# Performance work log

Hardware: AMD Instinct MI355X
Metric: run time of the kernel (lower is better)

The kernel has to match this reference:

```python
import jax, jax.numpy as jnp
import numpy as np

D = 256
H = 16
HD = D // H
N_BIAS = 6
B, E = 8, 1024


def _layernorm(x, g, b, eps=1e-5):
    mu = jnp.mean(x, axis=-1, keepdims=True)
    var = jnp.mean(jnp.square(x - mu), axis=-1, keepdims=True)
    return (x - mu) * jax.lax.rsqrt(var + eps) * g + b


def setup_inputs() -> dict:
    key = jax.random.key(0)
    ks = jax.random.split(key, 16)
    s = 0.02
    inp = {
        "x": jax.random.normal(ks[0], (B, E, D), dtype=jnp.float32),
        "struct_bias": jax.random.randint(ks[1], (B, E, E), 0, N_BIAS),
        "key_padding_mask": jnp.zeros((B, E), dtype=bool),
        # projections stored as [in, out] so y = x @ W + b
        "Wq": jax.random.normal(ks[2], (D, D), jnp.float32) * s,
        "bq": jnp.zeros((D,), jnp.float32),
        "Wk": jax.random.normal(ks[3], (D, D), jnp.float32) * s,
        "bk": jnp.zeros((D,), jnp.float32),
        "Wv": jax.random.normal(ks[4], (D, D), jnp.float32) * s,
        "bv": jnp.zeros((D,), jnp.float32),
        "Wo": jax.random.normal(ks[5], (D, D), jnp.float32) * s,
        "bo": jnp.zeros((D,), jnp.float32),
        "bias_emb": jax.random.normal(ks[6], (N_BIAS, H), jnp.float32) * s,
        "ln1_g": jnp.ones((D,), jnp.float32),
        "ln1_b": jnp.zeros((D,), jnp.float32),
        "W_ff1": jax.random.normal(ks[7], (D, 4 * D), jnp.float32) * s,
        "b_ff1": jnp.zeros((4 * D,), jnp.float32),
        "W_ff2": jax.random.normal(ks[8], (4 * D, D), jnp.float32) * s,
        "b_ff2": jnp.zeros((D,), jnp.float32),
        "ln2_g": jnp.ones((D,), jnp.float32),
        "ln2_b": jnp.zeros((D,), jnp.float32),
    }
    return inp


def reference(x, struct_bias, key_padding_mask, Wq, bq, Wk, bk, Wv, bv, Wo, bo,
              bias_emb, ln1_g, ln1_b, W_ff1, b_ff1, W_ff2, b_ff2, ln2_g, ln2_b):
    b, e, d = x.shape
    # project and split heads: [B, H, E, HD]
    q = (x @ Wq + bq).reshape(b, e, H, HD).transpose(0, 2, 1, 3)
    k = (x @ Wk + bk).reshape(b, e, H, HD).transpose(0, 2, 1, 3)
    v = (x @ Wv + bv).reshape(b, e, H, HD).transpose(0, 2, 1, 3)
    scores = jnp.einsum('bhqd,bhkd->bhqk', q, k) / np.sqrt(HD).astype(np.float32)
    # learned structural bias: [B,E,E,H] -> [B,H,E,E]
    bias = bias_emb[struct_bias].transpose(0, 3, 1, 2)
    scores = scores + bias
    scores = jnp.where(key_padding_mask[:, None, None, :], -jnp.inf, scores)
    attn = jax.nn.softmax(scores, axis=-1)
    out = jnp.einsum('bhqk,bhkd->bhqd', attn, v)
    out = out.transpose(0, 2, 1, 3).reshape(b, e, d)
    out = out @ Wo + bo
    x = _layernorm(x + out, ln1_g, ln1_b)
    ff = jax.nn.gelu(x @ W_ff1 + b_ff1, approximate=False) @ W_ff2 + b_ff2
    x = _layernorm(x + ff, ln2_g, ln2_b)
    return x
```

## Files before the change

### kernel.cpp

```cpp
#include <hip/hip_runtime.h>
#include <math.h>

#define B_  8
#define E_  1024
#define D_  256
#define H_  16
#define FF_ 1024
#define M_  (B_ * E_)

typedef __attribute__((ext_vector_type(8))) short short8;
typedef __attribute__((ext_vector_type(4))) float f32x4;
typedef unsigned short bf16u;

#define GLOAD_LDS16(g, l) __builtin_amdgcn_global_load_lds( \
    (const __attribute__((address_space(1))) void*)(g), \
    (__attribute__((address_space(3))) void*)(l), 16, 0, 0)

__device__ __forceinline__ unsigned short f2bf(float f) {
  union { float f; unsigned u; } c; c.f = f;
  unsigned r = c.u + 0x7fffu + ((c.u >> 16) & 1u);
  return (unsigned short)(r >> 16);
}
__device__ __forceinline__ float gelu_exact(float x) {
  return 0.5f * x * (1.0f + erff(x * 0.70710678118654752f));
}

template<int BM, int BN, int EPI>
__global__ __launch_bounds__(256) void mm_k(
    const bf16u* __restrict__ A, const bf16u* __restrict__ Wt,
    const float* __restrict__ bias, const float* __restrict__ R,
    void* __restrict__ Cout, int M, int N, int K)
{
  constexpr int WM = BM / 2, WN = BN / 2;
  constexpr int MT = WM / 16, NT = WN / 16;
  constexpr int PA = BM * 8 / 256, PB = BN * 8 / 256;
  constexpr int LBM = (BM == 128 ? 7 : 6), LBN = (BN == 128 ? 7 : 6);
  __shared__ bf16u As[BM * 64];
  __shared__ bf16u Bs[BN * 64];

  const int t = threadIdx.x;
  const int l15 = t & 15, quad = (t >> 4) & 3;
  const int w = t >> 6, wm = w >> 1, wn = w & 1;
  const int m0 = blockIdx.x * BM, n0 = blockIdx.y * BN;

  f32x4 acc[MT][NT];
  const f32x4 z4 = {0.f, 0.f, 0.f, 0.f};
#pragma unroll
  for (int i = 0; i < MT; ++i)
#pragma unroll
    for (int j = 0; j < NT; ++j) acc[i][j] = z4;

  for (int k0 = 0; k0 < K; k0 += 64) {
    __syncthreads();
#pragma unroll
    for (int p = 0; p < PA; ++p) {
      int g = p * 256 + t;
      int m = g & (BM - 1), c = g >> LBM;
      const bf16u* src = A + (size_t)(m0 + m) * K + k0 + c * 8;
      GLOAD_LDS16(src, As + g * 8);
    }
#pragma unroll
    for (int p = 0; p < PB; ++p) {
      int g = p * 256 + t;
      int n = g & (BN - 1), c = g >> LBN;
      const bf16u* src = Wt + (size_t)(n0 + n) * K + k0 + c * 8;
      GLOAD_LDS16(src, Bs + g * 8);
    }
    __syncthreads();
#pragma unroll
    for (int s = 0; s < 2; ++s) {
      short8 af[MT], bfr[NT];
#pragma unroll
      for (int mt = 0; mt < MT; ++mt)
        af[mt] = *(const short8*)(As + ((s * 4 + quad) * BM + wm * WM + mt * 16 + l15) * 8);
#pragma unroll
      for (int nt = 0; nt < NT; ++nt)
        bfr[nt] = *(const short8*)(Bs + ((s * 4 + quad) * BN + wn * WN + nt * 16 + l15) * 8);
#pragma unroll
      for (int mt = 0; mt < MT; ++mt)
#pragma unroll
        for (int nt = 0; nt < NT; ++nt)
          acc[mt][nt] = __builtin_amdgcn_mfma_f32_16x16x32_bf16(
              af[mt], bfr[nt], acc[mt][nt], 0, 0, 0);
    }
  }

#pragma unroll
  for (int mt = 0; mt < MT; ++mt) {
#pragma unroll
    for (int nt = 0; nt < NT; ++nt) {
      int col = n0 + wn * WN + nt * 16 + l15;
      float bia = bias[col];
#pragma unroll
      for (int r = 0; r < 4; ++r) {
        int row = m0 + wm * WM + mt * 16 + quad * 4 + r;
        size_t idx = (size_t)row * N + col;
        float v = acc[mt][nt][r] + bia;
        if (EPI == 1)      { ((float*)Cout)[idx] = v + R[idx]; }
        else if (EPI == 2) { ((bf16u*)Cout)[idx] = f2bf(gelu_exact(v)); }
        else               { ((bf16u*)Cout)[idx] = f2bf(v); }
      }
    }
  }
}

__global__ __launch_bounds__(256) void tcvt4_k(
    const float* __restrict__ s0, const float* __restrict__ s1,
    const float* __restrict__ s2, const float* __restrict__ s3,
    bf16u* __restrict__ d0, bf16u* __restrict__ d1,
    bf16u* __restrict__ d2, bf16u* __restrict__ d3)
{
  const int z = blockIdx.z;
  const float* src = (z == 0) ? s0 : (z == 1) ? s1 : (z == 2) ? s2 : s3;
  bf16u* dst = (z == 0) ? d0 : (z == 1) ? d1 : (z == 2) ? d2 : d3;
  __shared__ float tile[32][33];
  const int tx = threadIdx.x & 31, ty = threadIdx.x >> 5;
  const int kb = blockIdx.x * 32, nb = blockIdx.y * 32;
#pragma unroll
  for (int r = 0; r < 4; ++r)
    tile[ty + 8 * r][tx] = src[(size_t)(kb + ty + 8 * r) * 256 + nb + tx];
  __syncthreads();
#pragma unroll
  for (int r = 0; r < 4; ++r)
    dst[(size_t)(nb + ty + 8 * r) * 256 + kb + tx] = f2bf(tile[tx][ty + 8 * r]);
}

__global__ __launch_bounds__(256) void tcvt_k(const float* __restrict__ src,
    bf16u* __restrict__ dst, int K, int N)
{
  __shared__ float tile[32][33];
  const int tx = threadIdx.x & 31, ty = threadIdx.x >> 5;
  const int kb = blockIdx.x * 32, nb = blockIdx.y * 32;
#pragma unroll
  for (int r = 0; r < 4; ++r)
    tile[ty + 8 * r][tx] = src[(size_t)(kb + ty + 8 * r) * N + nb + tx];
  __syncthreads();
#pragma unroll
  for (int r = 0; r < 4; ++r)
    dst[(size_t)(nb + ty + 8 * r) * K + kb + tx] = f2bf(tile[tx][ty + 8 * r]);
}

__global__ __launch_bounds__(256) void cvt_k(const float* __restrict__ X,
    bf16u* __restrict__ Y)
{
  int i = blockIdx.x * 256 + threadIdx.x;
  float4 a = ((const float4*)X)[i * 2];
  float4 b = ((const float4*)X)[i * 2 + 1];
  uint4 o;
  o.x = f2bf(a.x) | ((unsigned)f2bf(a.y) << 16);
  o.y = f2bf(a.z) | ((unsigned)f2bf(a.w) << 16);
  o.z = f2bf(b.x) | ((unsigned)f2bf(b.y) << 16);
  o.w = f2bf(b.z) | ((unsigned)f2bf(b.w) << 16);
  ((uint4*)Y)[i] = o;
}

__global__ void bcat_k(const float* __restrict__ bq, const float* __restrict__ bk,
                       const float* __restrict__ bv, float* __restrict__ o)
{
  int i = blockIdx.x * 256 + threadIdx.x;
  o[i] = (i < 256) ? bq[i] : (i < 512) ? bk[i - 256] : bv[i - 512];
}

__global__ __launch_bounds__(256) void attn_k(
    const bf16u* __restrict__ qkv, const int* __restrict__ sb,
    const unsigned char* __restrict__ mask, const float* __restrict__ be,
    bf16u* __restrict__ O)
{
  __shared__ bf16u Kl[2][64][40];
  __shared__ bf16u Vt[2][16][72];
  __shared__ bf16u Pl[4][16][40];
  __shared__ float embl[2][6];

  const int t    = threadIdx.x;
  const int b    = blockIdx.z;
  const int hg   = blockIdx.y;
  const int w    = t >> 6;
  const int lane = t & 63;
  const int l15  = lane & 15;
  const int quad = lane >> 4;
  const int q0w  = blockIdx.x * 64 + w * 16;

  if (t < 12) embl[t / 6][t % 6] = be[(t % 6) * 16 + hg * 2 + t / 6];

  {
    float4 z = {0.f, 0.f, 0.f, 0.f};
    float4* kp = (float4*)&Kl[0][0][0];
    for (int i = t; i < 640; i += 256) kp[i] = z;
  }

  short8 qf[2];
#pragma unroll
  for (int hp = 0; hp < 2; ++hp) {
    uint4 v = {0u, 0u, 0u, 0u};
    if (quad < 2)
      v = *(const uint4*)(qkv + ((size_t)(b * E_) + q0w + l15) * 768 +
                          (hg * 2 + hp) * 16 + quad * 8);
    else if (quad == 2)
      v.x = 0x3F80u;
    union { uint4 u; short8 s; } c; c.u = v;
    qf[hp] = c.s;
  }

  const int s_hp   = t >> 7;
  const int s_key  = (t >> 1) & 63;
  const int s_half = t & 1;
  const size_t kvbase = (size_t)b * E_ * 768;
  const int* sbp = sb + ((size_t)b * E_ + q0w) * E_;

  f32x4 accO[2];
  const f32x4 z4 = {0.f, 0.f, 0.f, 0.f};
  accO[0] = z4; accO[1] = z4;
  float lsum[2][4] = {};

  for (int k0 = 0; k0 < E_; k0 += 64) {
    int sbv[2][2][4];
#pragma unroll
    for (int s2 = 0; s2 < 2; ++s2)
#pragma unroll
      for (int f = 0; f < 2; ++f)
#pragma unroll
        for (int r = 0; r < 4; ++r)
          sbv[s2][f][r] = sbp[(size_t)(quad * 4 + r) * E_ + k0 + s2 * 32 + f * 16 + l15];

    __syncthreads();
    {
      const bf16u* kq = qkv + kvbase + (size_t)(k0 + s_key) * 768 + 256 +
                        (hg * 2 + s_hp) * 16 + s_half * 8;
      uint4 kw = *(const uint4*)kq;
      uint4 vw = *(const uint4*)(kq + 256);
      *(uint4*)&Kl[s_hp][s_key][s_half * 8] = kw;
      const int col = (s_key >> 5) * 32 + ((s_key & 15) << 1) + ((s_key >> 4) & 1);
      union { uint4 u; bf16u e[8]; } vc; vc.u = vw;
#pragma unroll
      for (int j = 0; j < 8; ++j)
        Vt[s_hp][s_half * 8 + j][col] = vc.e[j];
      if (s_half == 0) {
        unsigned char mv = mask[b * E_ + k0 + s_key];
        Kl[s_hp][s_key][16] = mv ? (bf16u)0xCF6E : (bf16u)0;
      }
    }
    __syncthreads();

#pragma unroll
    for (int hp = 0; hp < 2; ++hp) {
#pragma unroll
      for (int s2 = 0; s2 < 2; ++s2) {
        short8 kf0 = *(const short8*)&Kl[hp][s2 * 32 + l15][quad * 8];
        short8 kf1 = *(const short8*)&Kl[hp][s2 * 32 + 16 + l15][quad * 8];
        f32x4 sc0 = __builtin_amdgcn_mfma_f32_16x16x32_bf16(qf[hp], kf0, z4, 0, 0, 0);
        f32x4 sc1 = __builtin_amdgcn_mfma_f32_16x16x32_bf16(qf[hp], kf1, z4, 0, 0, 0);
#pragma unroll
        for (int r = 0; r < 4; ++r) {
          float w0 = embl[hp][sbv[s2][0][r]];
          float w1 = embl[hp][sbv[s2][1][r]];
          float p0 = __expf(fmaf(sc0[r], 0.25f, w0));
          float p1 = __expf(fmaf(sc1[r], 0.25f, w1));
          unsigned u0 = __float_as_uint(p0) & 0xffff0000u;
          unsigned u1 = __float_as_uint(p1) & 0xffff0000u;
          lsum[hp][r] += __uint_as_float(u0) + __uint_as_float(u1);
          *(unsigned*)&Pl[w][quad * 4 + r][l15 * 2] = (__float_as_uint(p0) >> 16) | u1;
        }
        short8 pf = *(const short8*)&Pl[w][l15][quad * 8];
        short8 vf = *(const short8*)&Vt[hp][l15][s2 * 32 + quad * 8];
        accO[hp] = __builtin_amdgcn_mfma_f32_16x16x32_bf16(pf, vf, accO[hp], 0, 0, 0);
      }
    }
  }

#pragma unroll
  for (int off = 1; off <= 8; off <<= 1)
#pragma unroll
    for (int hp = 0; hp < 2; ++hp)
#pragma unroll
      for (int r = 0; r < 4; ++r)
        lsum[hp][r] += __shfl_xor(lsum[hp][r], off, 64);

#pragma unroll
  for (int hp = 0; hp < 2; ++hp) {
#pragma unroll
    for (int r = 0; r < 4; ++r) {
      float o = accO[hp][r] / lsum[hp][r];
      O[((size_t)(b * E_) + q0w + quad * 4 + r) * 256 + (hg * 2 + hp) * 16 + l15] = f2bf(o);
    }
  }
}

template<int DUAL>
__global__ __launch_bounds__(256) void ln_k(
    const float* __restrict__ X, const float* __restrict__ g,
    const float* __restrict__ bta, float* __restrict__ Y, bf16u* __restrict__ Yb)
{
  const int row  = blockIdx.x * 4 + (threadIdx.x >> 6);
  const int lane = threadIdx.x & 63;
  float4 v = *(const float4*)(X + (size_t)row * D_ + lane * 4);
  float s  = v.x + v.y + v.z + v.w;
  float ss = v.x * v.x + v.y * v.y + v.z * v.z + v.w * v.w;
#pragma unroll
  for (int off = 32; off; off >>= 1) {
    s  += __shfl_xor(s, off, 64);
    ss += __shfl_xor(ss, off, 64);
  }
  float mu  = s * (1.f / 256.f);
  float var = ss * (1.f / 256.f) - mu * mu;
  float rs  = 1.f / sqrtf(var + 1e-5f);
  float4 gv = *(const float4*)(g + lane * 4);
  float4 bv = *(const float4*)(bta + lane * 4);
  float4 o;
  o.x = (v.x - mu) * rs * gv.x + bv.x;
  o.y = (v.y - mu) * rs * gv.y + bv.y;
  o.z = (v.z - mu) * rs * gv.z + bv.z;
  o.w = (v.w - mu) * rs * gv.w + bv.w;
  *(float4*)(Y + (size_t)row * D_ + lane * 4) = o;
  if (DUAL) {
    uint2 p;
    p.x = f2bf(o.x) | ((unsigned)f2bf(o.y) << 16);
    p.y = f2bf(o.z) | ((unsigned)f2bf(o.w) << 16);
    *(uint2*)(Yb + (size_t)row * D_ + lane * 4) = p;
  }
}

extern "C" void kernel_launch(void* const* d_in, const int* in_sizes, int n_in,
                              void* d_out, int out_size, void* d_ws, size_t ws_size,
                              hipStream_t stream) {
  const float* x   = (const float*)d_in[0];
  const int*   sb  = (const int*)d_in[1];
  const unsigned char* mask = (const unsigned char*)d_in[2];
  const float* Wq  = (const float*)d_in[3];
  const float* bq  = (const float*)d_in[4];
  const float* Wk  = (const float*)d_in[5];
  const float* bk  = (const float*)d_in[6];
  const float* Wv  = (const float*)d_in[7];
  const float* bv  = (const float*)d_in[8];
  const float* Wo  = (const float*)d_in[9];
  const float* bo  = (const float*)d_in[10];
  const float* be  = (const float*)d_in[11];
  const float* g1  = (const float*)d_in[12];
  const float* b1  = (const float*)d_in[13];
  const float* Wf1 = (const float*)d_in[14];
  const float* bf1 = (const float*)d_in[15];
  const float* Wf2 = (const float*)d_in[16];
  const float* bf2 = (const float*)d_in[17];
  const float* g2  = (const float*)d_in[18];
  const float* b2  = (const float*)d_in[19];
  float* out = (float*)d_out;

  char* ws = (char*)d_ws;
  bf16u* Wqkvt = (bf16u*)(ws + 0);
  bf16u* Wot   = (bf16u*)(ws + 393216);
  bf16u* Wf1t  = (bf16u*)(ws + 524288);
  bf16u* Wf2t  = (bf16u*)(ws + 1048576);
  float* bqkv  = (float*)(ws + 1572864);
  bf16u* xb    = (bf16u*)(ws + 2097152);
  bf16u* qkv   = (bf16u*)(ws + 6291456);
  bf16u* att   = (bf16u*)(ws + 18874368);
  float* t1    = (float*)(ws + 23068672);
  float* x1    = (float*)(ws + 31457280);
  bf16u* x1b   = (bf16u*)(ws + 39845888);
  bf16u* ffh   = (bf16u*)(ws + 2097152);
  float* t2    = (float*)(ws + 18874368);

  dim3 blk(256);

  tcvt4_k<<<dim3(8, 8, 4), blk, 0, stream>>>(Wq, Wk, Wv, Wo,
      Wqkvt, Wqkvt + 65536, Wqkvt + 131072, Wot);
  tcvt_k<<<dim3(8, 32), blk, 0, stream>>>(Wf1, Wf1t, 256, 1024);
  tcvt_k<<<dim3(32, 8), blk, 0, stream>>>(Wf2, Wf2t, 1024, 256);
  bcat_k<<<3, blk, 0, stream>>>(bq, bk, bv, bqkv);
  cvt_k<<<1024, blk, 0, stream>>>(x, xb);

  mm_k<128, 128, 0><<<dim3(64, 6), blk, 0, stream>>>(xb, Wqkvt, bqkv, nullptr,
                                                     qkv, M_, 768, 256);
  attn_k<<<dim3(16, 8, 8), blk, 0, stream>>>(qkv, sb, mask, be, att);

  mm_k<64, 64, 1><<<dim3(128, 4), blk, 0, stream>>>(att, Wot, bo, x,
                                                    t1, M_, 256, 256);
  ln_k<1><<<M_ / 4, blk, 0, stream>>>(t1, g1, b1, x1, x1b);

  mm_k<128, 128, 2><<<dim3(64, 8), blk, 0, stream>>>(x1b, Wf1t, bf1, nullptr,
                                                     ffh, M_, 1024, 256);
  mm_k<64, 64, 1><<<dim3(128, 4), blk, 0, stream>>>(ffh, Wf2t, bf2, x1,
                                                    t2, M_, 256, 1024);
  ln_k<0><<<M_ / 4, blk, 0, stream>>>(t2, g2, b2, out, nullptr);
}
```

Measured before the change: 239.0 us.

## Pack struct bias to bytes, split attention per head, use exp2, retile QKV GEMM

A conversion pass now packs the int32 structural-bias indices into uint8, and the attention kernel reads those bytes. This cuts the dominant bias read traffic, which is otherwise repeated for every head group. The attention kernel now handles one head per block instead of two, which doubles the grid and shares K/V loading between thread halves. The exponent is folded into exp2 with prescaled constants. The QKV GEMM tile is halved in M. The one-head-per-block split means the bias bytes are re-read 16 times instead of 8, trading more repeated reads for more parallelism.

After: 248.2 us. 3.9% more time.

```diff
diff --git a/kernel.cpp b/kernel.cpp
--- a/kernel.cpp
+++ b/kernel.cpp
@@ -141,17 +141,29 @@
 }
 
 __global__ __launch_bounds__(256) void cvt_k(const float* __restrict__ X,
-    bf16u* __restrict__ Y)
-{
-  int i = blockIdx.x * 256 + threadIdx.x;
-  float4 a = ((const float4*)X)[i * 2];
-  float4 b = ((const float4*)X)[i * 2 + 1];
-  uint4 o;
-  o.x = f2bf(a.x) | ((unsigned)f2bf(a.y) << 16);
-  o.y = f2bf(a.z) | ((unsigned)f2bf(a.w) << 16);
-  o.z = f2bf(b.x) | ((unsigned)f2bf(b.y) << 16);
-  o.w = f2bf(b.z) | ((unsigned)f2bf(b.w) << 16);
-  ((uint4*)Y)[i] = o;
+    bf16u* __restrict__ Y, const int* __restrict__ sb,
+    unsigned char* __restrict__ sbb)
+{
+  const int bid = blockIdx.x;
+  if (bid < 1024) {
+    int i = bid * 256 + threadIdx.x;
+    float4 a = ((const float4*)X)[i * 2];
+    float4 b = ((const float4*)X)[i * 2 + 1];
+    uint4 o;
+    o.x = f2bf(a.x) | ((unsigned)f2bf(a.y) << 16);
+    o.y = f2bf(a.z) | ((unsigned)f2bf(a.w) << 16);
+    o.z = f2bf(b.x) | ((unsigned)f2bf(b.y) << 16);
+    o.w = f2bf(b.z) | ((unsigned)f2bf(b.w) << 16);
+    ((uint4*)Y)[i] = o;
+  } else {
+    int i = (bid - 1024) * 256 + threadIdx.x;
+    int4 a = ((const int4*)sb)[i * 2];
+    int4 c = ((const int4*)sb)[i * 2 + 1];
+    uint2 o;
+    o.x = (unsigned)a.x | ((unsigned)a.y << 8) | ((unsigned)a.z << 16) | ((unsigned)a.w << 24);
+    o.y = (unsigned)c.x | ((unsigned)c.y << 8) | ((unsigned)c.z << 16) | ((unsigned)c.w << 24);
+    ((uint2*)sbb)[i] = o;
+  }
 }
 
 __global__ void bcat_k(const float* __restrict__ bq, const float* __restrict__ bk,
@@ -162,55 +174,54 @@
 }
 
 __global__ __launch_bounds__(256) void attn_k(
-    const bf16u* __restrict__ qkv, const int* __restrict__ sb,
+    const bf16u* __restrict__ qkv, const unsigned char* __restrict__ sbb,
     const unsigned char* __restrict__ mask, const float* __restrict__ be,
     bf16u* __restrict__ O)
 {
-  __shared__ bf16u Kl[2][64][40];
-  __shared__ bf16u Vt[2][16][72];
+  __shared__ bf16u Kl[64][40];
+  __shared__ bf16u Vt[16][74];
   __shared__ bf16u Pl[4][16][40];
-  __shared__ float embl[2][6];
+  __shared__ float embl[6];
 
   const int t    = threadIdx.x;
   const int b    = blockIdx.z;
-  const int hg   = blockIdx.y;
+  const int h    = blockIdx.y;
   const int w    = t >> 6;
   const int lane = t & 63;
   const int l15  = lane & 15;
   const int quad = lane >> 4;
   const int q0w  = blockIdx.x * 64 + w * 16;
-
-  if (t < 12) embl[t / 6][t % 6] = be[(t % 6) * 16 + hg * 2 + t / 6];
+  const float C2 = 0.36067376022224085f;
+
+  if (t < 6) embl[t] = be[t * 16 + h] * 1.44269504088896f;
 
   {
     float4 z = {0.f, 0.f, 0.f, 0.f};
-    float4* kp = (float4*)&Kl[0][0][0];
-    for (int i = t; i < 640; i += 256) kp[i] = z;
-  }
-
-  short8 qf[2];
-#pragma unroll
-  for (int hp = 0; hp < 2; ++hp) {
+    float4* kp = (float4*)&Kl[0][0];
+    for (int i = t; i < 320; i += 256) kp[i] = z;
+  }
+
+  short8 qf;
+  {
     uint4 v = {0u, 0u, 0u, 0u};
     if (quad < 2)
       v = *(const uint4*)(qkv + ((size_t)(b * E_) + q0w + l15) * 768 +
-                          (hg * 2 + hp) * 16 + quad * 8);
+                          h * 16 + quad * 8);
     else if (quad == 2)
       v.x = 0x3F80u;
     union { uint4 u; short8 s; } c; c.u = v;
-    qf[hp] = c.s;
-  }
-
-  const int s_hp   = t >> 7;
+    qf = c.s;
+  }
+
   const int s_key  = (t >> 1) & 63;
   const int s_half = t & 1;
   const size_t kvbase = (size_t)b * E_ * 768;
-  const int* sbp = sb + ((size_t)b * E_ + q0w) * E_;
-
-  f32x4 accO[2];
+  const unsigned char* sbp = sbb + ((size_t)(b * E_) + q0w) * E_;
+
+  f32x4 accO;
   const f32x4 z4 = {0.f, 0.f, 0.f, 0.f};
-  accO[0] = z4; accO[1] = z4;
-  float lsum[2][4] = {};
+  accO = z4;
+  float lsum[4] = {};
 
   for (int k0 = 0; k0 < E_; k0 += 64) {
     int sbv[2][2][4];
@@ -224,64 +235,58 @@
 
     __syncthreads();
     {
-      const bf16u* kq = qkv + kvbase + (size_t)(k0 + s_key) * 768 + 256 +
-                        (hg * 2 + s_hp) * 16 + s_half * 8;
-      uint4 kw = *(const uint4*)kq;
-      uint4 vw = *(const uint4*)(kq + 256);
-      *(uint4*)&Kl[s_hp][s_key][s_half * 8] = kw;
-      const int col = (s_key >> 5) * 32 + ((s_key & 15) << 1) + ((s_key >> 4) & 1);
-      union { uint4 u; bf16u e[8]; } vc; vc.u = vw;
-#pragma unroll
-      for (int j = 0; j < 8; ++j)
-        Vt[s_hp][s_half * 8 + j][col] = vc.e[j];
-      if (s_half == 0) {
-        unsigned char mv = mask[b * E_ + k0 + s_key];
-        Kl[s_hp][s_key][16] = mv ? (bf16u)0xCF6E : (bf16u)0;
+      const bf16u* base = qkv + kvbase + (size_t)(k0 + s_key) * 768 +
+                          h * 16 + s_half * 8;
+      if (t < 128) {
+        *(uint4*)&Kl[s_key][s_half * 8] = *(const uint4*)(base + 256);
+        if (t < 64) {
+          unsigned char mv = mask[b * E_ + k0 + t];
+          Kl[t][16] = mv ? (bf16u)0xCF6E : (bf16u)0;
+        }
+      } else {
+        uint4 vw = *(const uint4*)(base + 512);
+        const int col = (s_key >> 5) * 32 + ((s_key & 15) << 1) + ((s_key >> 4) & 1);
+        union { uint4 u; bf16u e[8]; } vc; vc.u = vw;
+#pragma unroll
+        for (int j = 0; j < 8; ++j)
+          Vt[s_half * 8 + j][col] = vc.e[j];
       }
     }
     __syncthreads();
 
 #pragma unroll
-    for (int hp = 0; hp < 2; ++hp) {
-#pragma unroll
-      for (int s2 = 0; s2 < 2; ++s2) {
-        short8 kf0 = *(const short8*)&Kl[hp][s2 * 32 + l15][quad * 8];
-        short8 kf1 = *(const short8*)&Kl[hp][s2 * 32 + 16 + l15][quad * 8];
-        f32x4 sc0 = __builtin_amdgcn_mfma_f32_16x16x32_bf16(qf[hp], kf0, z4, 0, 0, 0);
-        f32x4 sc1 = __builtin_amdgcn_mfma_f32_16x16x32_bf16(qf[hp], kf1, z4, 0, 0, 0);
-#pragma unroll
-        for (int r = 0; r < 4; ++r) {
-          float w0 = embl[hp][sbv[s2][0][r]];
-          float w1 = embl[hp][sbv[s2][1][r]];
-          float p0 = __expf(fmaf(sc0[r], 0.25f, w0));
-          float p1 = __expf(fmaf(sc1[r], 0.25f, w1));
-          unsigned u0 = __float_as_uint(p0) & 0xffff0000u;
-          unsigned u1 = __float_as_uint(p1) & 0xffff0000u;
-          lsum[hp][r] += __uint_as_float(u0) + __uint_as_float(u1);
-          *(unsigned*)&Pl[w][quad * 4 + r][l15 * 2] = (__float_as_uint(p0) >> 16) | u1;
-        }
-        short8 pf = *(const short8*)&Pl[w][l15][quad * 8];
-        short8 vf = *(const short8*)&Vt[hp][l15][s2 * 32 + quad * 8];
-        accO[hp] = __builtin_amdgcn_mfma_f32_16x16x32_bf16(pf, vf, accO[hp], 0, 0, 0);
+    for (int s2 = 0; s2 < 2; ++s2) {
+      short8 kf0 = *(const short8*)&Kl[s2 * 32 + l15][quad * 8];
+      short8 kf1 = *(const short8*)&Kl[s2 * 32 + 16 + l15][quad * 8];
+      f32x4 sc0 = __builtin_amdgcn_mfma_f32_16x16x32_bf16(qf, kf0, z4, 0, 0, 0);
+      f32x4 sc1 = __builtin_amdgcn_mfma_f32_16x16x32_bf16(qf, kf1, z4, 0, 0, 0);
+#pragma unroll
+      for (int r = 0; r < 4; ++r) {
+        float w0 = embl[sbv[s2][0][r]];
+        float w1 = embl[sbv[s2][1][r]];
+        float p0 = __builtin_amdgcn_exp2f(fmaf(sc0[r], C2, w0));
+        float p1 = __builtin_amdgcn_exp2f(fmaf(sc1[r], C2, w1));
+        unsigned u0 = __float_as_uint(p0) & 0xffff0000u;
+        unsigned u1 = __float_as_uint(p1) & 0xffff0000u;
+        lsum[r] += __uint_as_float(u0) + __uint_as_float(u1);
+        *(unsigned*)&Pl[w][quad * 4 + r][l15 * 2] = (__float_as_uint(p0) >> 16) | u1;
       }
+      short8 pf = *(const short8*)&Pl[w][l15][quad * 8];
+      short8 vf = *(const short8*)&Vt[l15][s2 * 32 + quad * 8];
+      accO = __builtin_amdgcn_mfma_f32_16x16x32_bf16(pf, vf, accO, 0, 0, 0);
     }
   }
 
 #pragma unroll
   for (int off = 1; off <= 8; off <<= 1)
 #pragma unroll
-    for (int hp = 0; hp < 2; ++hp)
-#pragma unroll
-      for (int r = 0; r < 4; ++r)
-        lsum[hp][r] += __shfl_xor(lsum[hp][r], off, 64);
-
-#pragma unroll
-  for (int hp = 0; hp < 2; ++hp) {
-#pragma unroll
-    for (int r = 0; r < 4; ++r) {
-      float o = accO[hp][r] / lsum[hp][r];
-      O[((size_t)(b * E_) + q0w + quad * 4 + r) * 256 + (hg * 2 + hp) * 16 + l15] = f2bf(o);
-    }
+    for (int r = 0; r < 4; ++r)
+      lsum[r] += __shfl_xor(lsum[r], off, 64);
+
+#pragma unroll
+  for (int r = 0; r < 4; ++r) {
+    float o = accO[r] / lsum[r];
+    O[((size_t)(b * E_) + q0w + quad * 4 + r) * 256 + h * 16 + l15] = f2bf(o);
   }
 }
 
@@ -353,6 +358,7 @@
   bf16u* xb    = (bf16u*)(ws + 2097152);
   bf16u* qkv   = (bf16u*)(ws + 6291456);
   bf16u* att   = (bf16u*)(ws + 18874368);
+  unsigned char* sbb = (unsigned char*)(ws + 23068672);
   float* t1    = (float*)(ws + 23068672);
   float* x1    = (float*)(ws + 31457280);
   bf16u* x1b   = (bf16u*)(ws + 39845888);
@@ -366,11 +372,11 @@
   tcvt_k<<<dim3(8, 32), blk, 0, stream>>>(Wf1, Wf1t, 256, 1024);
   tcvt_k<<<dim3(32, 8), blk, 0, stream>>>(Wf2, Wf2t, 1024, 256);
   bcat_k<<<3, blk, 0, stream>>>(bq, bk, bv, bqkv);
-  cvt_k<<<1024, blk, 0, stream>>>(x, xb);
-
-  mm_k<128, 128, 0><<<dim3(64, 6), blk, 0, stream>>>(xb, Wqkvt, bqkv, nullptr,
+  cvt_k<<<5120, blk, 0, stream>>>(x, xb, sb, sbb);
+
+  mm_k<64, 128, 0><<<dim3(128, 6), blk, 0, stream>>>(xb, Wqkvt, bqkv, nullptr,
                                                      qkv, M_, 768, 256);
-  attn_k<<<dim3(16, 8, 8), blk, 0, stream>>>(qkv, sb, mask, be, att);
+  attn_k<<<dim3(16, 16, 8), blk, 0, stream>>>(qkv, sbb, mask, be, att);
 
   mm_k<64, 64, 1><<<dim3(128, 4), blk, 0, stream>>>(att, Wot, bo, x,
                                                     t1, M_, 256, 256);
```

## Fuse prep kernels, pack struct bias to bytes, double-buffer attention K/V loads

Applied to the files above, without the earlier changes.

Merges the five small weight/bias/input conversion kernels into one prep kernel, which also packs the int32 structural-bias indices into bytes so the attention kernel reads a quarter of the bytes for the dominant B*E*E stream. The attention loop becomes register-prefetched and double-buffered in LDS with one barrier per iteration. It also folds log2e into the scale and embeddings to use exp2, swizzles K in LDS, pads V, and sets a min-blocks launch bound. The packing pass adds a full read of the int32 index tensor each call, the larger LDS footprint may reduce occupancy, and the byte buffer reuses workspace later used for t1.

Measured after the change: 316.4 us. 32.4% more time.

```diff
diff --git a/kernel.cpp b/kernel.cpp
--- a/kernel.cpp
+++ b/kernel.cpp
@@ -104,70 +104,76 @@
   }
 }
 
-__global__ __launch_bounds__(256) void tcvt4_k(
-    const float* __restrict__ s0, const float* __restrict__ s1,
-    const float* __restrict__ s2, const float* __restrict__ s3,
-    bf16u* __restrict__ d0, bf16u* __restrict__ d1,
-    bf16u* __restrict__ d2, bf16u* __restrict__ d3)
-{
-  const int z = blockIdx.z;
-  const float* src = (z == 0) ? s0 : (z == 1) ? s1 : (z == 2) ? s2 : s3;
-  bf16u* dst = (z == 0) ? d0 : (z == 1) ? d1 : (z == 2) ? d2 : d3;
-  __shared__ float tile[32][33];
-  const int tx = threadIdx.x & 31, ty = threadIdx.x >> 5;
-  const int kb = blockIdx.x * 32, nb = blockIdx.y * 32;
-#pragma unroll
-  for (int r = 0; r < 4; ++r)
-    tile[ty + 8 * r][tx] = src[(size_t)(kb + ty + 8 * r) * 256 + nb + tx];
-  __syncthreads();
-#pragma unroll
-  for (int r = 0; r < 4; ++r)
-    dst[(size_t)(nb + ty + 8 * r) * 256 + kb + tx] = f2bf(tile[tx][ty + 8 * r]);
-}
-
-__global__ __launch_bounds__(256) void tcvt_k(const float* __restrict__ src,
-    bf16u* __restrict__ dst, int K, int N)
+__global__ __launch_bounds__(256) void prep_k(
+    const float* __restrict__ Wq, const float* __restrict__ Wk,
+    const float* __restrict__ Wv, const float* __restrict__ Wo,
+    const float* __restrict__ Wf1, const float* __restrict__ Wf2,
+    bf16u* __restrict__ Wqkvt, bf16u* __restrict__ Wot,
+    bf16u* __restrict__ Wf1t, bf16u* __restrict__ Wf2t,
+    const float* __restrict__ bq, const float* __restrict__ bk,
+    const float* __restrict__ bv, float* __restrict__ bqkv,
+    const float* __restrict__ X, bf16u* __restrict__ Xb,
+    const int* __restrict__ sb, unsigned char* __restrict__ sbb)
 {
   __shared__ float tile[32][33];
-  const int tx = threadIdx.x & 31, ty = threadIdx.x >> 5;
-  const int kb = blockIdx.x * 32, nb = blockIdx.y * 32;
-#pragma unroll
-  for (int r = 0; r < 4; ++r)
-    tile[ty + 8 * r][tx] = src[(size_t)(kb + ty + 8 * r) * N + nb + tx];
-  __syncthreads();
-#pragma unroll
-  for (int r = 0; r < 4; ++r)
-    dst[(size_t)(nb + ty + 8 * r) * K + kb + tx] = f2bf(tile[tx][ty + 8 * r]);
-}
-
-__global__ __launch_bounds__(256) void cvt_k(const float* __restrict__ X,
-    bf16u* __restrict__ Y)
-{
-  int i = blockIdx.x * 256 + threadIdx.x;
-  float4 a = ((const float4*)X)[i * 2];
-  float4 b = ((const float4*)X)[i * 2 + 1];
-  uint4 o;
-  o.x = f2bf(a.x) | ((unsigned)f2bf(a.y) << 16);
-  o.y = f2bf(a.z) | ((unsigned)f2bf(a.w) << 16);
-  o.z = f2bf(b.x) | ((unsigned)f2bf(b.y) << 16);
-  o.w = f2bf(b.z) | ((unsigned)f2bf(b.w) << 16);
-  ((uint4*)Y)[i] = o;
-}
-
-__global__ void bcat_k(const float* __restrict__ bq, const float* __restrict__ bk,
-                       const float* __restrict__ bv, float* __restrict__ o)
-{
-  int i = blockIdx.x * 256 + threadIdx.x;
-  o[i] = (i < 256) ? bq[i] : (i < 512) ? bk[i - 256] : bv[i - 512];
-}
-
-__global__ __launch_bounds__(256) void attn_k(
-    const bf16u* __restrict__ qkv, const int* __restrict__ sb,
+  const int gid = blockIdx.x;
+  const int t = threadIdx.x;
+
+  if (gid < 768) {
+    const float* src; bf16u* dst; int K, N, bx, by;
+    if (gid < 256) {
+      const int z = gid >> 6, r = gid & 63;
+      src = (z == 0) ? Wq : (z == 1) ? Wk : (z == 2) ? Wv : Wo;
+      dst = (z == 0) ? Wqkvt : (z == 1) ? Wqkvt + 65536
+          : (z == 2) ? Wqkvt + 131072 : Wot;
+      K = 256; N = 256; bx = r & 7; by = r >> 3;
+    } else if (gid < 512) {
+      const int r = gid - 256;
+      src = Wf1; dst = Wf1t; K = 256; N = 1024; bx = r & 7; by = r >> 3;
+    } else {
+      const int r = gid - 512;
+      src = Wf2; dst = Wf2t; K = 1024; N = 256; bx = r & 31; by = r >> 5;
+    }
+    const int tx = t & 31, ty = t >> 5;
+    const int kb = bx * 32, nb = by * 32;
+#pragma unroll
+    for (int r = 0; r < 4; ++r)
+      tile[ty + 8 * r][tx] = src[(size_t)(kb + ty + 8 * r) * N + nb + tx];
+    __syncthreads();
+#pragma unroll
+    for (int r = 0; r < 4; ++r)
+      dst[(size_t)(nb + ty + 8 * r) * K + kb + tx] = f2bf(tile[tx][ty + 8 * r]);
+  } else if (gid < 771) {
+    int i = (gid - 768) * 256 + t;
+    bqkv[i] = (i < 256) ? bq[i] : (i < 512) ? bk[i - 256] : bv[i - 512];
+  } else if (gid < 1795) {
+    int i = (gid - 771) * 256 + t;
+    float4 a = ((const float4*)X)[i * 2];
+    float4 b = ((const float4*)X)[i * 2 + 1];
+    uint4 o;
+    o.x = f2bf(a.x) | ((unsigned)f2bf(a.y) << 16);
+    o.y = f2bf(a.z) | ((unsigned)f2bf(a.w) << 16);
+    o.z = f2bf(b.x) | ((unsigned)f2bf(b.y) << 16);
+    o.w = f2bf(b.z) | ((unsigned)f2bf(b.w) << 16);
+    ((uint4*)Xb)[i] = o;
+  } else {
+    int i = (gid - 1795) * 256 + t;
+    int4 a = ((const int4*)sb)[i * 2];
+    int4 c = ((const int4*)sb)[i * 2 + 1];
+    uint2 o;
+    o.x = (unsigned)a.x | ((unsigned)a.y << 8) | ((unsigned)a.z << 16) | ((unsigned)a.w << 24);
+    o.y = (unsigned)c.x | ((unsigned)c.y << 8) | ((unsigned)c.z << 16) | ((unsigned)c.w << 24);
+    ((uint2*)sbb)[i] = o;
+  }
+}
+
+__global__ __launch_bounds__(256, 4) void attn_k(
+    const bf16u* __restrict__ qkv, const unsigned char* __restrict__ sbb,
     const unsigned char* __restrict__ mask, const float* __restrict__ be,
     bf16u* __restrict__ O)
 {
-  __shared__ bf16u Kl[2][64][40];
-  __shared__ bf16u Vt[2][16][72];
+  __shared__ bf16u Kl[2][2][64][40];
+  __shared__ bf16u Vt[2][2][16][74];
   __shared__ bf16u Pl[4][16][40];
   __shared__ float embl[2][6];
 
@@ -179,13 +185,14 @@
   const int l15  = lane & 15;
   const int quad = lane >> 4;
   const int q0w  = blockIdx.x * 64 + w * 16;
-
-  if (t < 12) embl[t / 6][t % 6] = be[(t % 6) * 16 + hg * 2 + t / 6];
+  const float C2 = 0.36067376022224085f;
+
+  if (t < 12) embl[t / 6][t % 6] = be[(t % 6) * 16 + hg * 2 + t / 6] * 1.44269504088896f;
 
   {
     float4 z = {0.f, 0.f, 0.f, 0.f};
-    float4* kp = (float4*)&Kl[0][0][0];
-    for (int i = t; i < 640; i += 256) kp[i] = z;
+    float4* kp = (float4*)&Kl[0][0][0][0];
+    for (int i = t; i < 1280; i += 256) kp[i] = z;
   }
 
   short8 qf[2];
@@ -205,65 +212,100 @@
   const int s_key  = (t >> 1) & 63;
   const int s_half = t & 1;
   const size_t kvbase = (size_t)b * E_ * 768;
-  const int* sbp = sb + ((size_t)b * E_ + q0w) * E_;
+  const unsigned char* sbp = sbb + ((size_t)(b * E_) + q0w) * E_;
+  const bf16u* kqbase = qkv + kvbase + 256 + (hg * 2 + s_hp) * 16 + s_half * 8;
+
+  const int wroff = (s_half * 8) ^ (((s_key >> 3) & 1) << 3);
+  const int koff  = (quad < 2) ? ((quad * 8) ^ ((l15 >> 3) << 3)) : (quad * 8);
+  const int vcol  = ((s_key >> 5) << 5) + ((s_key & 15) << 1) + ((s_key >> 4) & 1);
 
   f32x4 accO[2];
   const f32x4 z4 = {0.f, 0.f, 0.f, 0.f};
   accO[0] = z4; accO[1] = z4;
   float lsum[2][4] = {};
 
-  for (int k0 = 0; k0 < E_; k0 += 64) {
-    int sbv[2][2][4];
+  uint4 kA, vA; unsigned mA = 0; int sA[2][2][4];
+  {
+    const bf16u* p = kqbase + (size_t)s_key * 768;
+    kA = *(const uint4*)p;
+    vA = *(const uint4*)(p + 256);
+    if (s_half == 0) mA = mask[b * E_ + s_key];
 #pragma unroll
     for (int s2 = 0; s2 < 2; ++s2)
 #pragma unroll
       for (int f = 0; f < 2; ++f)
 #pragma unroll
         for (int r = 0; r < 4; ++r)
-          sbv[s2][f][r] = sbp[(size_t)(quad * 4 + r) * E_ + k0 + s2 * 32 + f * 16 + l15];
+          sA[s2][f][r] = sbp[(size_t)(quad * 4 + r) * E_ + s2 * 32 + f * 16 + l15];
+  }
+  __syncthreads();
+
+#pragma unroll 2
+  for (int i = 0; i < 16; ++i) {
+    const int cur = i & 1;
+
+    *(uint4*)&Kl[cur][s_hp][s_key][wroff] = kA;
+    {
+      union { uint4 u; bf16u e[8]; } vc; vc.u = vA;
+#pragma unroll
+      for (int j = 0; j < 8; ++j)
+        Vt[cur][s_hp][s_half * 8 + j][vcol] = vc.e[j];
+    }
+    if (s_half == 0)
+      Kl[cur][s_hp][s_key][16] = mA ? (bf16u)0xCF6E : (bf16u)0;
+
+    uint4 kB, vB; unsigned mB = 0; int sB[2][2][4];
+    if (i < 15) {
+      const int kn = (i + 1) * 64;
+      const bf16u* p = kqbase + (size_t)(kn + s_key) * 768;
+      kB = *(const uint4*)p;
+      vB = *(const uint4*)(p + 256);
+      if (s_half == 0) mB = mask[b * E_ + kn + s_key];
+#pragma unroll
+      for (int s2 = 0; s2 < 2; ++s2)
+#pragma unroll
+        for (int f = 0; f < 2; ++f)
+#pragma unroll
+          for (int r = 0; r < 4; ++r)
+            sB[s2][f][r] = sbp[(size_t)(quad * 4 + r) * E_ + kn + s2 * 32 + f * 16 + l15];
+    }
 
     __syncthreads();
-    {
-      const bf16u* kq = qkv + kvbase + (size_t)(k0 + s_key) * 768 + 256 +
-                        (hg * 2 + s_hp) * 16 + s_half * 8;
-      uint4 kw = *(const uint4*)kq;
-      uint4 vw = *(const uint4*)(kq + 256);
-      *(uint4*)&Kl[s_hp][s_key][s_half * 8] = kw;
-      const int col = (s_key >> 5) * 32 + ((s_key & 15) << 1) + ((s_key >> 4) & 1);
-      union { uint4 u; bf16u e[8]; } vc; vc.u = vw;
-#pragma unroll
-      for (int j = 0; j < 8; ++j)
-        Vt[s_hp][s_half * 8 + j][col] = vc.e[j];
-      if (s_half == 0) {
-        unsigned char mv = mask[b * E_ + k0 + s_key];
-        Kl[s_hp][s_key][16] = mv ? (bf16u)0xCF6E : (bf16u)0;
-      }
-    }
-    __syncthreads();
 
 #pragma unroll
     for (int hp = 0; hp < 2; ++hp) {
 #pragma unroll
       for (int s2 = 0; s2 < 2; ++s2) {
-        short8 kf0 = *(const short8*)&Kl[hp][s2 * 32 + l15][quad * 8];
-        short8 kf1 = *(const short8*)&Kl[hp][s2 * 32 + 16 + l15][quad * 8];
+        short8 kf0 = *(const short8*)&Kl[cur][hp][s2 * 32 + l15][koff];
+        short8 kf1 = *(const short8*)&Kl[cur][hp][s2 * 32 + 16 + l15][koff];
         f32x4 sc0 = __builtin_amdgcn_mfma_f32_16x16x32_bf16(qf[hp], kf0, z4, 0, 0, 0);
         f32x4 sc1 = __builtin_amdgcn_mfma_f32_16x16x32_bf16(qf[hp], kf1, z4, 0, 0, 0);
 #pragma unroll
         for (int r = 0; r < 4; ++r) {
-          float w0 = embl[hp][sbv[s2][0][r]];
-          float w1 = embl[hp][sbv[s2][1][r]];
-          float p0 = __expf(fmaf(sc0[r], 0.25f, w0));
-          float p1 = __expf(fmaf(sc1[r], 0.25f, w1));
+          float w0 = embl[hp][sA[s2][0][r]];
+          float w1 = embl[hp][sA[s2][1][r]];
+          float p0 = __builtin_amdgcn_exp2f(fmaf(sc0[r], C2, w0));
+          float p1 = __builtin_amdgcn_exp2f(fmaf(sc1[r], C2, w1));
           unsigned u0 = __float_as_uint(p0) & 0xffff0000u;
           unsigned u1 = __float_as_uint(p1) & 0xffff0000u;
           lsum[hp][r] += __uint_as_float(u0) + __uint_as_float(u1);
           *(unsigned*)&Pl[w][quad * 4 + r][l15 * 2] = (__float_as_uint(p0) >> 16) | u1;
         }
         short8 pf = *(const short8*)&Pl[w][l15][quad * 8];
-        short8 vf = *(const short8*)&Vt[hp][l15][s2 * 32 + quad * 8];
+        short8 vf = *(const short8*)&Vt[cur][hp][l15][s2 * 32 + quad * 8];
         accO[hp] = __builtin_amdgcn_mfma_f32_16x16x32_bf16(pf, vf, accO[hp], 0, 0, 0);
       }
+    }
+
+    if (i < 15) {
+      kA = kB; vA = vB; mA = mB;
+#pragma unroll
+      for (int s2 = 0; s2 < 2; ++s2)
+#pragma unroll
+        for (int f = 0; f < 2; ++f)
+#pragma unroll
+          for (int r = 0; r < 4; ++r)
+            sA[s2][f][r] = sB[s2][f][r];
     }
   }
 
@@ -353,6 +395,7 @@
   bf16u* xb    = (bf16u*)(ws + 2097152);
   bf16u* qkv   = (bf16u*)(ws + 6291456);
   bf16u* att   = (bf16u*)(ws + 18874368);
+  unsigned char* sbb = (unsigned char*)(ws + 23068672);
   float* t1    = (float*)(ws + 23068672);
   float* x1    = (float*)(ws + 31457280);
   bf16u* x1b   = (bf16u*)(ws + 39845888);
@@ -361,16 +404,13 @@
 
   dim3 blk(256);
 
-  tcvt4_k<<<dim3(8, 8, 4), blk, 0, stream>>>(Wq, Wk, Wv, Wo,
-      Wqkvt, Wqkvt + 65536, Wqkvt + 131072, Wot);
-  tcvt_k<<<dim3(8, 32), blk, 0, stream>>>(Wf1, Wf1t, 256, 1024);
-  tcvt_k<<<dim3(32, 8), blk, 0, stream>>>(Wf2, Wf2t, 1024, 256);
-  bcat_k<<<3, blk, 0, stream>>>(bq, bk, bv, bqkv);
-  cvt_k<<<1024, blk, 0, stream>>>(x, xb);
+  prep_k<<<5891, blk, 0, stream>>>(Wq, Wk, Wv, Wo, Wf1, Wf2,
+                                   Wqkvt, Wot, Wf1t, Wf2t,
+                                   bq, bk, bv, bqkv, x, xb, sb, sbb);
 
   mm_k<128, 128, 0><<<dim3(64, 6), blk, 0, stream>>>(xb, Wqkvt, bqkv, nullptr,
                                                      qkv, M_, 768, 256);
-  attn_k<<<dim3(16, 8, 8), blk, 0, stream>>>(qkv, sb, mask, be, att);
+  attn_k<<<dim3(16, 8, 8), blk, 0, stream>>>(qkv, sbb, mask, be, att);
 
   mm_k<64, 64, 1><<<dim3(128, 4), blk, 0, stream>>>(att, Wot, bo, x,
                                                     t1, M_, 256, 256);
```
